# Optimization experiments

Hardware: AMD Instinct MI355X
Metric: run time of the kernel (lower is better)

## Reference

```python
import jax, jax.numpy as jnp
import numpy as np

ALPHA = 8.3  # depth similarity sharpness, F_D = exp(-alpha*|D(p0)-D(pn)|) (depth-aware CNN)
PAD, STRIDE, DIL, KH, KW = 1, 1, 1, 3, 3


def setup_inputs() -> dict:
    key = jax.random.key(0)
    k1, k2, k3, k4 = jax.random.split(key, 4)
    B, C_in, C_out, H, W = 2, 32, 32, 512, 512
    x = jax.random.normal(k1, (B, C_in, H, W), dtype=jnp.float32)
    depth = jax.random.uniform(k2, (B, 1, H, W), dtype=jnp.float32)
    weight = jax.random.normal(k3, (C_out, C_in, KH, KW), dtype=jnp.float32) * 0.05
    bias = jax.random.normal(k4, (C_out,), dtype=jnp.float32) * 0.05
    return {"x": x, "depth": depth, "weight": weight, "bias": bias}


def _depthconv(x, depth, weight, bias):
    B, C, H, W = x.shape
    C_out = weight.shape[0]
    H_out = (H + 2 * PAD - DIL * (KH - 1) - 1) // STRIDE + 1
    W_out = (W + 2 * PAD - DIL * (KW - 1) - 1) // STRIDE + 1
    x_p = jnp.pad(x, ((0, 0), (0, 0), (PAD, PAD), (PAD, PAD)))
    d_p = jnp.pad(depth, ((0, 0), (0, 0), (PAD, PAD), (PAD, PAD)))
    # depth at the receptive-field center of each output pixel, [B,1,H_out,W_out]
    ci, cj = (KH // 2) * DIL, (KW // 2) * DIL
    d_c = d_p[:, :, ci:ci + H_out * STRIDE:STRIDE, cj:cj + W_out * STRIDE:STRIDE]
    out = jnp.broadcast_to(bias[None, :, None, None], (B, C_out, H_out, W_out)).astype(x.dtype)
    for ki in range(KH):
        for kj in range(KW):
            hs, ws = ki * DIL, kj * DIL
            xs = x_p[:, :, hs:hs + H_out * STRIDE:STRIDE, ws:ws + W_out * STRIDE:STRIDE]
            ds = d_p[:, :, hs:hs + H_out * STRIDE:STRIDE, ws:ws + W_out * STRIDE:STRIDE]
            sim = jnp.exp(-ALPHA * jnp.abs(d_c - ds))  # [B,1,H_out,W_out]
            out = out + jnp.einsum('oc,bchw->bohw', weight[:, :, ki, kj], xs * sim)
    return out


def reference(x, depth, weight, bias):
    return _depthconv(x, depth, weight, bias)
```

## Files before the change

### kernel.cpp

```cpp
#include <hip/hip_runtime.h>

typedef _Float16 half8 __attribute__((ext_vector_type(8)));
typedef float floatx4 __attribute__((ext_vector_type(4)));

constexpr int C  = 32, H = 512, W = 512, HW = H * W;
constexpr int Hp = 514, Wp = 514;
constexpr int NPX = 2 * Hp * Wp;

constexpr size_t XOFF = 0;
constexpr size_t XSZ  = (size_t)NPX * 64;
constexpr size_t DOFF = XOFF + XSZ;
constexpr size_t DSZ  = (size_t)NPX * 8;
constexpr size_t WOFF = DOFF + DSZ;

__device__ __forceinline__ unsigned pack2h(float lo, float hi) {
    unsigned a = (unsigned)__builtin_bit_cast(unsigned short, (_Float16)lo);
    unsigned b = (unsigned)__builtin_bit_cast(unsigned short, (_Float16)hi);
    return a | (b << 16);
}

__global__ __launch_bounds__(256) void pack_all(
    const float* __restrict__ x, const float* __restrict__ depth,
    const float* __restrict__ weight,
    unsigned* __restrict__ xp, float2* __restrict__ dpk, uint4* __restrict__ wp)
{
    const int bid = blockIdx.x;
    const int tid = threadIdx.x;

    if (bid >= 2048) {
        if (bid < 2065) {
            int i = (bid - 2048) * 256 + tid;
            if (i >= 4104) return;
            int b = i / 2052, r = i % 2052;
            int hh, ww;
            if (r < 514)       { hh = 0;   ww = r; }
            else if (r < 1028) { hh = 513; ww = r - 514; }
            else { int j = r - 1028; hh = 1 + (j >> 1); ww = (j & 1) ? 513 : 0; }
            size_t ppx = ((size_t)(b * Hp + hh)) * Wp + ww;
            uint4 z = {0u, 0u, 0u, 0u};
            uint4* p = (uint4*)(xp + ppx * 16);
            p[0] = z; p[1] = z; p[2] = z; p[3] = z;
            dpk[ppx] = make_float2(0.f, 0.f);
        } else {
            int j = (bid - 2065) * 256 + tid;
            if (j >= 1152) return;
            int lane = j & 63, half = (j >> 6) & 1, tap = j >> 7;
            int o = half * 16 + (lane & 15), q = lane >> 4;
            uint4 v;
            v.x = pack2h(weight[(o * 32 + q * 8 + 0) * 9 + tap], weight[(o * 32 + q * 8 + 1) * 9 + tap]);
            v.y = pack2h(weight[(o * 32 + q * 8 + 2) * 9 + tap], weight[(o * 32 + q * 8 + 3) * 9 + tap]);
            v.z = pack2h(weight[(o * 32 + q * 8 + 4) * 9 + tap], weight[(o * 32 + q * 8 + 5) * 9 + tap]);
            v.w = pack2h(weight[(o * 32 + q * 8 + 6) * 9 + tap], weight[(o * 32 + q * 8 + 7) * 9 + tap]);
            wp[j] = v;
        }
        return;
    }

    __shared__ float t[4][32][65];
    const int wseg = bid & 7, hseg = (bid >> 3) & 127, b = bid >> 10;
    const int h0 = hseg * 4, w0 = wseg * 64;

    const float* xb = x + (size_t)b * C * HW + h0 * W + w0;
    #pragma unroll
    for (int p = 0; p < 8; ++p) {
        int slot = p * 256 + tid;
        int r = slot >> 9, c = (slot >> 4) & 31, f4 = slot & 15;
        float4 v = *(const float4*)(xb + (size_t)c * HW + r * W + f4 * 4);
        t[r][c][f4 * 4 + 0] = v.x; t[r][c][f4 * 4 + 1] = v.y;
        t[r][c][f4 * 4 + 2] = v.z; t[r][c][f4 * 4 + 3] = v.w;
    }

    {
        int rr = tid >> 6, ww = tid & 63;
        float d = depth[(size_t)b * HW + (h0 + rr) * W + w0 + ww];
        size_t ppx = ((size_t)(b * Hp + h0 + rr + 1)) * Wp + (w0 + 1 + ww);
        dpk[ppx] = make_float2(__expf(-8.3f * d), __expf(8.3f * d));
    }
    __syncthreads();

    const int px = tid >> 2, q = tid & 3;
    #pragma unroll
    for (int r = 0; r < 4; ++r) {
        uint4 o;
        o.x = pack2h(t[r][q * 8 + 0][px], t[r][q * 8 + 1][px]);
        o.y = pack2h(t[r][q * 8 + 2][px], t[r][q * 8 + 3][px]);
        o.z = pack2h(t[r][q * 8 + 4][px], t[r][q * 8 + 5][px]);
        o.w = pack2h(t[r][q * 8 + 6][px], t[r][q * 8 + 7][px]);
        size_t ppx = ((size_t)(b * Hp + h0 + r + 1)) * Wp + (w0 + 1 + px);
        *(uint4*)(xp + ppx * 16 + q * 4) = o;
    }
}

__global__ __launch_bounds__(256) void depthconv_main(
    const unsigned* __restrict__ xp,
    const float2*   __restrict__ dpk,
    const uint4*    __restrict__ wp,
    const float*    __restrict__ bias,
    float*          __restrict__ out)
{
    const int bid  = blockIdx.x;
    const int wseg = bid & 7, h = (bid >> 3) & 511, b = bid >> 12;
    const int lane = threadIdx.x & 63, wid = threadIdx.x >> 6;
    const int nn   = lane & 15, q = lane >> 4;
    const int pw   = wseg * 64 + wid * 16 + nn;

    half8 af[2][9];
    #pragma unroll
    for (int tap = 0; tap < 9; ++tap) {
        af[0][tap] = __builtin_bit_cast(half8, wp[(tap * 2 + 0) * 64 + lane]);
        af[1][tap] = __builtin_bit_cast(half8, wp[(tap * 2 + 1) * 64 + lane]);
    }

    floatx4 acc0, acc1;
    #pragma unroll
    for (int r = 0; r < 4; ++r) {
        acc0[r] = bias[q * 4 + r];
        acc1[r] = bias[16 + q * 4 + r];
    }

    const size_t rowbase = ((size_t)(b * Hp + h)) * Wp + pw;
    const float2 dc = dpk[rowbase + Wp + 1];

    #pragma unroll
    for (int ki = 0; ki < 3; ++ki) {
        #pragma unroll
        for (int kj = 0; kj < 3; ++kj) {
            const int tap = ki * 3 + kj;
            const size_t np = rowbase + (size_t)ki * Wp + kj;
            float2 dn = dpk[np];
            float s = fminf(dn.y * dc.x, dn.x * dc.y);
            _Float16 hs = (_Float16)s;
            half8 sv = { hs, hs, hs, hs, hs, hs, hs, hs };

            half8 xv = __builtin_bit_cast(half8, *(const uint4*)(xp + np * 16 + q * 4));
            half8 bfrag = xv * sv;

            acc0 = __builtin_amdgcn_mfma_f32_16x16x32_f16(af[0][tap], bfrag, acc0, 0, 0, 0);
            acc1 = __builtin_amdgcn_mfma_f32_16x16x32_f16(af[1][tap], bfrag, acc1, 0, 0, 0);
        }
    }

    float* op = out + (size_t)b * C * HW + h * W + pw;
    #pragma unroll
    for (int r = 0; r < 4; ++r) {
        op[(size_t)(q * 4 + r) * HW]        = acc0[r];
        op[(size_t)(16 + q * 4 + r) * HW]   = acc1[r];
    }
}

extern "C" void kernel_launch(void* const* d_in, const int* in_sizes, int n_in,
                              void* d_out, int out_size, void* d_ws, size_t ws_size,
                              hipStream_t stream) {
    const float* x      = (const float*)d_in[0];
    const float* depth  = (const float*)d_in[1];
    const float* weight = (const float*)d_in[2];
    const float* bias   = (const float*)d_in[3];
    float* out          = (float*)d_out;

    unsigned* xp  = (unsigned*)((char*)d_ws + XOFF);
    float2*   dpk = (float2*)  ((char*)d_ws + DOFF);
    uint4*    wpk = (uint4*)   ((char*)d_ws + WOFF);

    hipLaunchKernelGGL(pack_all, dim3(2070), dim3(256), 0, stream,
                       x, depth, weight, xp, dpk, wpk);
    hipLaunchKernelGGL(depthconv_main, dim3(2 * 512 * 8), dim3(256), 0, stream,
                       xp, dpk, wpk, bias, out);
}
```

Measured before the change: 160.1 us.

## Retile pack kernel by row halves and hoist all neighbor loads before MFMAs

New measurement: 163.4 us. 2.0% more time.

```diff
diff --git a/kernel.cpp b/kernel.cpp
--- a/kernel.cpp
+++ b/kernel.cpp
@@ -12,6 +12,8 @@
 constexpr size_t DOFF = XOFF + XSZ;
 constexpr size_t DSZ  = (size_t)NPX * 8;
 constexpr size_t WOFF = DOFF + DSZ;
+
+constexpr int PITCH = 258;
 
 __device__ __forceinline__ unsigned pack2h(float lo, float hi) {
     unsigned a = (unsigned)__builtin_bit_cast(unsigned short, (_Float16)lo);
@@ -56,37 +58,40 @@
         return;
     }
 
-    __shared__ float t[4][32][65];
-    const int wseg = bid & 7, hseg = (bid >> 3) & 127, b = bid >> 10;
-    const int h0 = hseg * 4, w0 = wseg * 64;
+    __shared__ float t[32][PITCH];
+    const int halfrow = bid & 1, h = (bid >> 1) & 511, b = bid >> 10;
+    const int px0 = halfrow * 256;
 
-    const float* xb = x + (size_t)b * C * HW + h0 * W + w0;
+    const float* xb = x + (size_t)b * C * HW + h * W + px0;
+    const int c = tid >> 3, f = tid & 7;
+    float4 v[8];
     #pragma unroll
-    for (int p = 0; p < 8; ++p) {
-        int slot = p * 256 + tid;
-        int r = slot >> 9, c = (slot >> 4) & 31, f4 = slot & 15;
-        float4 v = *(const float4*)(xb + (size_t)c * HW + r * W + f4 * 4);
-        t[r][c][f4 * 4 + 0] = v.x; t[r][c][f4 * 4 + 1] = v.y;
-        t[r][c][f4 * 4 + 2] = v.z; t[r][c][f4 * 4 + 3] = v.w;
+    for (int i = 0; i < 8; ++i)
+        v[i] = *(const float4*)(xb + (size_t)c * HW + (f + 8 * i) * 4);
+    #pragma unroll
+    for (int i = 0; i < 8; ++i) {
+        int px = (f + 8 * i) * 4;
+        *(float2*)&t[c][px]     = make_float2(v[i].x, v[i].y);
+        *(float2*)&t[c][px + 2] = make_float2(v[i].z, v[i].w);
     }
 
     {
-        int rr = tid >> 6, ww = tid & 63;
-        float d = depth[(size_t)b * HW + (h0 + rr) * W + w0 + ww];
-        size_t ppx = ((size_t)(b * Hp + h0 + rr + 1)) * Wp + (w0 + 1 + ww);
+        float d = depth[(size_t)b * HW + h * W + px0 + tid];
+        size_t ppx = ((size_t)(b * Hp + h + 1)) * Wp + (px0 + 1 + tid);
         dpk[ppx] = make_float2(__expf(-8.3f * d), __expf(8.3f * d));
     }
     __syncthreads();
 
-    const int px = tid >> 2, q = tid & 3;
+    const int q = tid & 3;
     #pragma unroll
     for (int r = 0; r < 4; ++r) {
+        int px = r * 64 + (tid >> 2);
         uint4 o;
-        o.x = pack2h(t[r][q * 8 + 0][px], t[r][q * 8 + 1][px]);
-        o.y = pack2h(t[r][q * 8 + 2][px], t[r][q * 8 + 3][px]);
-        o.z = pack2h(t[r][q * 8 + 4][px], t[r][q * 8 + 5][px]);
-        o.w = pack2h(t[r][q * 8 + 6][px], t[r][q * 8 + 7][px]);
-        size_t ppx = ((size_t)(b * Hp + h0 + r + 1)) * Wp + (w0 + 1 + px);
+        o.x = pack2h(t[q * 8 + 0][px], t[q * 8 + 1][px]);
+        o.y = pack2h(t[q * 8 + 2][px], t[q * 8 + 3][px]);
+        o.z = pack2h(t[q * 8 + 4][px], t[q * 8 + 5][px]);
+        o.w = pack2h(t[q * 8 + 6][px], t[q * 8 + 7][px]);
+        size_t ppx = ((size_t)(b * Hp + h + 1)) * Wp + (px0 + 1 + px);
         *(uint4*)(xp + ppx * 16 + q * 4) = o;
     }
 }
@@ -104,11 +109,19 @@
     const int nn   = lane & 15, q = lane >> 4;
     const int pw   = wseg * 64 + wid * 16 + nn;
 
-    half8 af[2][9];
+    const size_t rowbase = ((size_t)(b * Hp + h)) * Wp + pw;
+
+    uint4  xv[9];
+    float2 dn[9];
     #pragma unroll
-    for (int tap = 0; tap < 9; ++tap) {
-        af[0][tap] = __builtin_bit_cast(half8, wp[(tap * 2 + 0) * 64 + lane]);
-        af[1][tap] = __builtin_bit_cast(half8, wp[(tap * 2 + 1) * 64 + lane]);
+    for (int ki = 0; ki < 3; ++ki) {
+        #pragma unroll
+        for (int kj = 0; kj < 3; ++kj) {
+            const int tap = ki * 3 + kj;
+            const size_t np = rowbase + (size_t)ki * Wp + kj;
+            xv[tap] = *(const uint4*)(xp + np * 16 + q * 4);
+            dn[tap] = dpk[np];
+        }
     }
 
     floatx4 acc0, acc1;
@@ -118,33 +131,28 @@
         acc1[r] = bias[16 + q * 4 + r];
     }
 
-    const size_t rowbase = ((size_t)(b * Hp + h)) * Wp + pw;
-    const float2 dc = dpk[rowbase + Wp + 1];
+    const float2 dc = dn[4];
 
     #pragma unroll
-    for (int ki = 0; ki < 3; ++ki) {
-        #pragma unroll
-        for (int kj = 0; kj < 3; ++kj) {
-            const int tap = ki * 3 + kj;
-            const size_t np = rowbase + (size_t)ki * Wp + kj;
-            float2 dn = dpk[np];
-            float s = fminf(dn.y * dc.x, dn.x * dc.y);
-            _Float16 hs = (_Float16)s;
-            half8 sv = { hs, hs, hs, hs, hs, hs, hs, hs };
+    for (int tap = 0; tap < 9; ++tap) {
+        float s = (tap == 4) ? 1.0f
+                             : fminf(dn[tap].y * dc.x, dn[tap].x * dc.y);
+        _Float16 hs = (_Float16)s;
+        half8 sv = { hs, hs, hs, hs, hs, hs, hs, hs };
+        half8 bfrag = __builtin_bit_cast(half8, xv[tap]) * sv;
 
-            half8 xv = __builtin_bit_cast(half8, *(const uint4*)(xp + np * 16 + q * 4));
-            half8 bfrag = xv * sv;
+        half8 af0 = __builtin_bit_cast(half8, wp[(tap * 2 + 0) * 64 + lane]);
+        half8 af1 = __builtin_bit_cast(half8, wp[(tap * 2 + 1) * 64 + lane]);
 
-            acc0 = __builtin_amdgcn_mfma_f32_16x16x32_f16(af[0][tap], bfrag, acc0, 0, 0, 0);
-            acc1 = __builtin_amdgcn_mfma_f32_16x16x32_f16(af[1][tap], bfrag, acc1, 0, 0, 0);
-        }
+        acc0 = __builtin_amdgcn_mfma_f32_16x16x32_f16(af0, bfrag, acc0, 0, 0, 0);
+        acc1 = __builtin_amdgcn_mfma_f32_16x16x32_f16(af1, bfrag, acc1, 0, 0, 0);
     }
 
     float* op = out + (size_t)b * C * HW + h * W + pw;
     #pragma unroll
     for (int r = 0; r < 4; ++r) {
-        op[(size_t)(q * 4 + r) * HW]        = acc0[r];
-        op[(size_t)(16 + q * 4 + r) * HW]   = acc1[r];
+        __builtin_nontemporal_store(acc0[r], op + (size_t)(q * 4 + r) * HW);
+        __builtin_nontemporal_store(acc1[r], op + (size_t)(16 + q * 4 + r) * HW);
     }
 }
 
```
